# Kernel tuning notes

Measured on AMD Instinct MI355X. Metric: run time of the kernel, lower is better.

## Reference

```python
import jax, jax.numpy as jnp
import numpy as np

N = 128          # number of nodes (particles)
NR = N * (N - 1) # number of directed edges, receiver-major order
B = 128          # batch
C = 16           # channel dim


def setup_inputs() -> dict:
    key = jax.random.key(0)
    x = jax.random.normal(key, (B, NR, C), dtype=jnp.float32)
    # assign_matrices enumerates (r, s) pairs receiver-major, so edge i has
    # receiver i // (N-1); Rr2 is the one-hot indicator of this mapping.
    receivers = jnp.arange(NR, dtype=jnp.int32) // (N - 1)
    return {"x": x, "receivers": receivers}


def reference(x, receivers):
    # exp of edge scores
    e = jnp.exp(x)  # [B, Nr, C]
    # tensordot(exp, Rr2, axes=[1,1]) == segment-sum over edges grouped by receiver
    seg = jax.ops.segment_sum(e.transpose(1, 0, 2), receivers, num_segments=N)  # [N, B, C]
    # tensordot(exp_sum, Rr2, axes=1) == gather each edge's receiver sum back to edges
    denom = seg[receivers]                 # [Nr, B, C]
    denom = denom.transpose(1, 2, 0)       # [B, C, Nr]
    # NOTE: the original divides the raw inputs (not exp) by the summed exp
    return x.transpose(0, 2, 1) / denom    # [B, C, Nr]
```

## Files before the change

### kernel.cpp

```cpp
#include <hip/hip_runtime.h>

#define NN   128
#define NE   127
#define CH   16
#define NRE  (NN * NE)
#define RPB  4
#define EPB  (RPB * NE)
#define F4PB (EPB * CH / 4)

__global__ __launch_bounds__(256, 4)
void attn2_kernel(const float* __restrict__ x, float* __restrict__ out) {
    __shared__ __align__(16) float T[CH][EPB];
    __shared__ float4 P[4][RPB][4];
    __shared__ float  R[RPB][CH];

    const int tid = threadIdx.x;
    const int w   = tid >> 6;
    const int t   = tid & 63;
    const int cg  = tid & 3;
    const int e0  = tid >> 2;

    const int b   = blockIdx.x >> 5;
    const int chk = blockIdx.x & 31;

    const float4* xs4 = (const float4*)(x + ((size_t)b * NRE + (size_t)chk * EPB) * CH);

    float4 v[8];
    #pragma unroll
    for (int it = 0; it < 8; ++it) {
        int f = tid + (it << 8);
        v[it] = xs4[f < F4PB ? f : F4PB - 1];
    }

    float4 acc[RPB];
    #pragma unroll
    for (int r = 0; r < RPB; ++r) acc[r] = float4{0.f, 0.f, 0.f, 0.f};

    const int c0 = cg << 2;
    #pragma unroll
    for (int it = 0; it < 8; ++it) {
        int f = tid + (it << 8);
        if (f < F4PB) {
            int e = e0 + (it << 6);
            T[c0 + 0][e] = v[it].x;
            T[c0 + 1][e] = v[it].y;
            T[c0 + 2][e] = v[it].z;
            T[c0 + 3][e] = v[it].w;
            float ex = __expf(v[it].x), ey = __expf(v[it].y);
            float ez = __expf(v[it].z), ew = __expf(v[it].w);
            const int m = it >> 1;
            if ((it & 1) == 0) {
                acc[m].x += ex; acc[m].y += ey; acc[m].z += ez; acc[m].w += ew;
            } else if (it == 7) {
                acc[3].x += ex; acc[3].y += ey; acc[3].z += ez; acc[3].w += ew;
            } else if (e0 < 63 - m) {
                acc[m].x += ex; acc[m].y += ey; acc[m].z += ez; acc[m].w += ew;
            } else {
                acc[m + 1].x += ex; acc[m + 1].y += ey;
                acc[m + 1].z += ez; acc[m + 1].w += ew;
            }
        }
    }

    #pragma unroll
    for (int msk = 4; msk <= 32; msk <<= 1) {
        #pragma unroll
        for (int r = 0; r < RPB; ++r) {
            acc[r].x += __shfl_xor(acc[r].x, msk, 64);
            acc[r].y += __shfl_xor(acc[r].y, msk, 64);
            acc[r].z += __shfl_xor(acc[r].z, msk, 64);
            acc[r].w += __shfl_xor(acc[r].w, msk, 64);
        }
    }
    if (t < 4) {
        #pragma unroll
        for (int r = 0; r < RPB; ++r) P[w][r][t] = acc[r];
    }
    __syncthreads();

    if (tid < 64) {
        int r = tid >> 4, c = tid & 15, j = c & 3;
        const float* p0 = (const float*)&P[0][r][c >> 2];
        const float* p1 = (const float*)&P[1][r][c >> 2];
        const float* p2 = (const float*)&P[2][r][c >> 2];
        const float* p3 = (const float*)&P[3][r][c >> 2];
        R[r][c] = 1.0f / (p0[j] + p1[j] + p2[j] + p3[j]);
    }
    __syncthreads();

    float* ob = out + (size_t)b * CH * NRE + (size_t)chk * EPB;
    #pragma unroll
    for (int it = 0; it < 8; ++it) {
        int f2 = tid + (it << 8);
        if (f2 < F4PB) {
            int c = f2 / NE;
            int m = f2 - c * NE;
            int e = m << 2;
            const float4 val = *(const float4*)&T[c][e];
            float4 o;
            o.x = val.x * R[(e + 0) / NE][c];
            o.y = val.y * R[(e + 1) / NE][c];
            o.z = val.z * R[(e + 2) / NE][c];
            o.w = val.w * R[(e + 3) / NE][c];
            *(float4*)(ob + (size_t)c * NRE + e) = o;
        }
    }
}

extern "C" void kernel_launch(void* const* d_in, const int* in_sizes, int n_in,
                              void* d_out, int out_size, void* d_ws, size_t ws_size,
                              hipStream_t stream) {
    const float* x = (const float*)d_in[0];
    float* out = (float*)d_out;
    attn2_kernel<<<128 * 32, 256, 0, stream>>>(x, out);
}
```

Baseline: 235.1 us.

## Load input directly into swizzled LDS and transpose output via cross-lane shuffles

Replaces the register-staged global loads and per-channel scalar LDS transpose with `global_load_lds` DMA into a float4 LDS buffer. The buffer uses an XOR-style rotation swizzle to avoid bank conflicts. The output phase reads float4 rows back from LDS, scales them by per-receiver reciprocals, and does a 4x4 transpose across lanes with `__shfl_xor` before issuing coalesced float4 stores. This aims to cut VGPR pressure, scalar LDS stores and bank conflicts, in exchange for an explicit vmcnt wait and extra shuffle instructions.

Measured after the change: 236.2 us. No clear change (+0.5%).

```diff
diff --git a/kernel.cpp b/kernel.cpp
--- a/kernel.cpp
+++ b/kernel.cpp
@@ -6,48 +6,52 @@
 #define NRE  (NN * NE)
 #define RPB  4
 #define EPB  (RPB * NE)
-#define F4PB (EPB * CH / 4)
+#define GPB  (EPB * CH / 4)
+#define GALL 2048
 
 __global__ __launch_bounds__(256, 4)
 void attn2_kernel(const float* __restrict__ x, float* __restrict__ out) {
-    __shared__ __align__(16) float T[CH][EPB];
+    __shared__ __align__(16) float4 L[GALL];
     __shared__ float4 P[4][RPB][4];
-    __shared__ float  R[RPB][CH];
+    __shared__ float4 R4[RPB][4];
 
     const int tid = threadIdx.x;
     const int w   = tid >> 6;
     const int t   = tid & 63;
-    const int cg  = tid & 3;
-    const int e0  = tid >> 2;
 
     const int b   = blockIdx.x >> 5;
     const int chk = blockIdx.x & 31;
 
     const float4* xs4 = (const float4*)(x + ((size_t)b * NRE + (size_t)chk * EPB) * CH);
 
-    float4 v[8];
+    typedef __attribute__((address_space(1))) const void GV;
+    typedef __attribute__((address_space(3))) void LV;
     #pragma unroll
     for (int it = 0; it < 8; ++it) {
-        int f = tid + (it << 8);
-        v[it] = xs4[f < F4PB ? f : F4PB - 1];
+        int f   = tid + (it << 8);
+        int fc  = f < GPB ? f : GPB - 1;
+        int e   = fc >> 2;
+        int src = (fc & ~3) | ((fc - e) & 3);
+        __builtin_amdgcn_global_load_lds((GV*)(const void*)(xs4 + src),
+                                         (LV*)(void*)&L[(it << 8) + (w << 6)],
+                                         16, 0, 0);
     }
+    asm volatile("s_waitcnt vmcnt(0)" ::: "memory");
+    __syncthreads();
 
+    const int e0 = tid >> 2;
+    const int g  = tid & 3;
     float4 acc[RPB];
     #pragma unroll
     for (int r = 0; r < RPB; ++r) acc[r] = float4{0.f, 0.f, 0.f, 0.f};
 
-    const int c0 = cg << 2;
     #pragma unroll
     for (int it = 0; it < 8; ++it) {
-        int f = tid + (it << 8);
-        if (f < F4PB) {
-            int e = e0 + (it << 6);
-            T[c0 + 0][e] = v[it].x;
-            T[c0 + 1][e] = v[it].y;
-            T[c0 + 2][e] = v[it].z;
-            T[c0 + 3][e] = v[it].w;
-            float ex = __expf(v[it].x), ey = __expf(v[it].y);
-            float ez = __expf(v[it].z), ew = __expf(v[it].w);
+        int e = e0 + (it << 6);
+        if (e < EPB) {
+            float4 v = L[(e << 2) | ((g + e) & 3)];
+            float ex = __expf(v.x), ey = __expf(v.y);
+            float ez = __expf(v.z), ew = __expf(v.w);
             const int m = it >> 1;
             if ((it & 1) == 0) {
                 acc[m].x += ex; acc[m].y += ey; acc[m].z += ez; acc[m].w += ew;
@@ -77,32 +81,43 @@
         for (int r = 0; r < RPB; ++r) P[w][r][t] = acc[r];
     }
     __syncthreads();
-
     if (tid < 64) {
-        int r = tid >> 4, c = tid & 15, j = c & 3;
-        const float* p0 = (const float*)&P[0][r][c >> 2];
-        const float* p1 = (const float*)&P[1][r][c >> 2];
-        const float* p2 = (const float*)&P[2][r][c >> 2];
-        const float* p3 = (const float*)&P[3][r][c >> 2];
-        R[r][c] = 1.0f / (p0[j] + p1[j] + p2[j] + p3[j]);
+        int r = tid >> 4, c = tid & 15, cg = c >> 2, j = c & 3;
+        const float* p0 = (const float*)&P[0][r][cg];
+        const float* p1 = (const float*)&P[1][r][cg];
+        const float* p2 = (const float*)&P[2][r][cg];
+        const float* p3 = (const float*)&P[3][r][cg];
+        ((float*)&R4[r][cg])[j] = 1.0f / (p0[j] + p1[j] + p2[j] + p3[j]);
     }
     __syncthreads();
 
     float* ob = out + (size_t)b * CH * NRE + (size_t)chk * EPB;
+    const int a = t >> 2;
+    const int q = t & 3;
     #pragma unroll
-    for (int it = 0; it < 8; ++it) {
-        int f2 = tid + (it << 8);
-        if (f2 < F4PB) {
-            int c = f2 / NE;
-            int m = f2 - c * NE;
-            int e = m << 2;
-            const float4 val = *(const float4*)&T[c][e];
-            float4 o;
-            o.x = val.x * R[(e + 0) / NE][c];
-            o.y = val.y * R[(e + 1) / NE][c];
-            o.z = val.z * R[(e + 2) / NE][c];
-            o.w = val.w * R[(e + 3) / NE][c];
-            *(float4*)(ob + (size_t)c * NRE + e) = o;
+    for (int j = 0; j < 8; ++j) {
+        const int G  = j & 3;
+        const int E0 = ((j >> 2) << 8) | (w << 6);
+        int e  = E0 + t;
+        int er = e < EPB ? e : EPB - 1;
+        float4 v = L[(er << 2) | ((G + er) & 3)];
+        int r = er / NE;
+        float4 rc = R4[r][G];
+        v.x *= rc.x; v.y *= rc.y; v.z *= rc.z; v.w *= rc.w;
+        float s0 = (q & 1) ? v.x : v.y;
+        float s1 = (q & 1) ? v.z : v.w;
+        s0 = __shfl_xor(s0, 1, 64);
+        s1 = __shfl_xor(s1, 1, 64);
+        if (q & 1) { v.x = s0; v.z = s1; } else { v.y = s0; v.w = s1; }
+        float u0 = (q & 2) ? v.x : v.z;
+        float u1 = (q & 2) ? v.y : v.w;
+        u0 = __shfl_xor(u0, 2, 64);
+        u1 = __shfl_xor(u1, 2, 64);
+        if (q & 2) { v.x = u0; v.y = u1; } else { v.z = u0; v.w = u1; }
+        const int eb = E0 + (a << 2);
+        if (eb < EPB) {
+            const int c = (G << 2) | q;
+            *(float4*)(ob + (size_t)c * NRE + eb) = v;
         }
     }
 }
```
